# Kernel tuning notes

Measured on AMD Instinct MI355X. Metric: run time of the kernel, lower is better.

## Reference

```python
import jax, jax.numpy as jnp
import numpy as np

B, N, K = 4, 4096, 16
C_IN = 128
EPS = 1e-5


def setup_inputs() -> dict:
    key = jax.random.key(0)
    ks = jax.random.split(key, 8)
    c0 = 2 * C_IN + 3  # concat channels: pos_diff(3) + feat2(128) + feat1(128)
    return {
        "pos1": jax.random.normal(ks[0], (B, 3, N), jnp.float32),
        "pos2": jax.random.normal(ks[1], (B, 3, N), jnp.float32),
        "feature1": jax.random.normal(ks[2], (B, C_IN, N), jnp.float32),
        "feature2": jax.random.normal(ks[3], (B, C_IN, N), jnp.float32),
        "W0": jax.random.normal(ks[4], (128, c0), jnp.float32) * 0.05,
        "W1": jax.random.normal(ks[5], (128, 128), jnp.float32) * 0.05,
        "W2": jax.random.normal(ks[6], (128, 128), jnp.float32) * 0.05,
        "g0": jnp.ones((128,), jnp.float32),
        "g1": jnp.ones((128,), jnp.float32),
        "g2": jnp.ones((128,), jnp.float32),
        "b0": jnp.zeros((128,), jnp.float32),
        "b1": jnp.zeros((128,), jnp.float32),
        "b2": jnp.zeros((128,), jnp.float32),
    }


def _knn_idx(pos1, pos2, k):
    # pos1, pos2: (B, 3, N).  For each point in pos1, k nearest points in pos2.
    p1 = pos1.transpose(0, 2, 1)  # (B, N, 3)
    p2 = pos2.transpose(0, 2, 1)  # (B, M, 3)
    d = (jnp.sum(p1 * p1, -1, keepdims=True)
         + jnp.sum(p2 * p2, -1)[:, None, :]
         - 2.0 * jnp.einsum("bnc,bmc->bnm", p1, p2))  # (B, N, M) squared dists
    _, idx = jax.lax.top_k(-d, k)  # (B, N, K)
    return idx


def _group(x, idx):
    # x: (B, C, M), idx: (B, N, K) -> (B, C, N, K)
    xt = x.transpose(0, 2, 1)  # (B, M, C)
    g = jax.vmap(lambda a, i: a[i])(xt, idx)  # (B, N, K, C)
    return g.transpose(0, 3, 1, 2)


def _conv_bn_relu(x, W, g, b):
    # 1x1 conv (no bias) + BatchNorm2d (training: batch stats, biased var) + ReLU
    y = jnp.einsum("oc,bcnk->bonk", W, x)
    mu = jnp.mean(y, axis=(0, 2, 3), keepdims=True)
    var = jnp.var(y, axis=(0, 2, 3), keepdims=True)
    yn = (y - mu) * jax.lax.rsqrt(var + EPS)
    return jax.nn.relu(yn * g[None, :, None, None] + b[None, :, None, None])


def reference(pos1, pos2, feature1, feature2, W0, W1, W2, g0, g1, g2, b0, b1, b2):
    idx = _knn_idx(pos1, pos2, K)                      # (B, N, K)
    pos2_g = _group(pos2, idx)                         # (B, 3, N, K)
    pos_diff = pos2_g - pos1[:, :, :, None]
    feat2_g = _group(feature2, idx)                    # (B, C, N, K)
    feat1_rep = jnp.broadcast_to(feature1[:, :, :, None], (B, C_IN, N, K))
    x = jnp.concatenate([pos_diff, feat2_g, feat1_rep], axis=1)  # (B, 2C+3, N, K)
    x = _conv_bn_relu(x, W0, g0, b0)
    x = _conv_bn_relu(x, W1, g1, b1)
    x = _conv_bn_relu(x, W2, g2, b2)
    feat1_new = jnp.max(x, axis=-1)                    # (B, mlp[-1], N)
    return (pos1, feat1_new)
```

## Files before the change

kernel.cpp:

```cpp
#include <hip/hip_runtime.h>

#define B_ 4
#define N_ 4096
#define K_ 16
#define C_ 128
#define NQ (B_*N_)
#define COLS_TOT (NQ*K_)
#define CNT_F 262144.0f
#define EPS_ 1e-5f

typedef __attribute__((ext_vector_type(8))) short short8;
typedef __attribute__((ext_vector_type(4))) float f4;
typedef __attribute__((ext_vector_type(4))) int i4;
typedef unsigned long long u64;

__device__ __forceinline__ unsigned short f2bf(float f){
  unsigned u = __builtin_bit_cast(unsigned, f);
  u = u + 0x7fffu + ((u >> 16) & 1u);
  return (unsigned short)(u >> 16);
}
__device__ __forceinline__ float bf2f(unsigned short h){
  return __builtin_bit_cast(float, ((unsigned)h) << 16);
}
__device__ __forceinline__ int swzc(int c){ return c ^ ((c >> 3) & 7); }

__global__ __launch_bounds__(256) void knn_wconv(
    const float* __restrict__ pos1, const float* __restrict__ pos2,
    u64* __restrict__ kout,
    const float* __restrict__ W0, const float* __restrict__ W1,
    const float* __restrict__ W2,
    unsigned short* __restrict__ W0b, unsigned short* __restrict__ W0c,
    unsigned short* __restrict__ W1b, unsigned short* __restrict__ W2b)
{
  if (blockIdx.x >= 1024){
    int i = (blockIdx.x - 1024) * 256 + threadIdx.x;
    int sel = i >> 14, r = i & 16383;
    int o = r >> 7, c = r & 127;
    float v; unsigned short* dst;
    if (sel == 0)      { v = W0[o*259 + 3   + c]; dst = W0b; }
    else if (sel == 1) { v = W0[o*259 + 131 + c]; dst = W0c; }
    else if (sel == 2) { v = W1[o*128 + c];       dst = W1b; }
    else               { v = W2[o*128 + c];       dst = W2b; }
    dst[r] = f2bf(v);
    return;
  }
  __shared__ __align__(16) float pts[256*4];
  int bx = blockIdx.x;
  int b = bx >> 8, rest = bx & 255, ngrp = rest >> 4, chunk = rest & 15;
  int t = threadIdx.x;
  int m0 = chunk * 256;
  const float* p2 = pos2 + (size_t)b*3*N_;
  {
    int m = m0 + t;
    float x = p2[m], y = p2[N_ + m], z = p2[2*N_ + m];
    float sq = __fadd_rn(__fadd_rn(__fmul_rn(x,x), __fmul_rn(y,y)), __fmul_rn(z,z));
    f4 v; v.x = x; v.y = y; v.z = z; v.w = sq;
    *(f4*)(pts + t*4) = v;
  }
  __syncthreads();

  int n = ngrp*256 + t;
  const float* p1 = pos1 + (size_t)b*3*N_;
  float qx = p1[n], qy = p1[N_ + n], qz = p1[2*N_ + n];
  float qs = __fadd_rn(__fadd_rn(__fmul_rn(qx,qx), __fmul_rn(qy,qy)), __fmul_rn(qz,qz));

  u64 list[16];
  #pragma unroll
  for (int j = 0; j < 16; ++j) list[j] = ~0ull;

  #pragma unroll 1
  for (int tile = 0; tile < 16; ++tile){
    u64 tk[16];
    #pragma unroll
    for (int e = 0; e < 16; ++e){
      int it = tile*16 + e;
      f4 c = *(const f4*)(pts + it*4);
      float dot = __builtin_fmaf(qz, c.z,
                    __builtin_fmaf(qy, c.y, __fmul_rn(qx, c.x)));
      float d = __fsub_rn(__fadd_rn(qs, c.w), __fmul_rn(2.0f, dot));
      d = __fadd_rn(d, 0.0f);
      unsigned u = __builtin_bit_cast(unsigned, d);
      u ^= (unsigned)((int)u >> 31) | 0x80000000u;
      tk[e] = ((u64)u << 32) | (unsigned)(m0 + it);
    }
    #pragma unroll
    for (int k = 2; k <= 16; k <<= 1)
      #pragma unroll
      for (int j2 = k >> 1; j2 > 0; j2 >>= 1)
        #pragma unroll
        for (int i = 0; i < 16; ++i){
          int l = i ^ j2;
          if (l > i){
            bool up = ((i & k) == 0);
            u64 a = tk[i], bb = tk[l];
            bool sw = up ? (a > bb) : (a < bb);
            u64 lo = sw ? bb : a, hi = sw ? a : bb;
            tk[i] = lo; tk[l] = hi;
          }
        }
    u64 m16[16];
    #pragma unroll
    for (int i = 0; i < 16; ++i){
      u64 a = list[i], bb = tk[15 - i];
      m16[i] = a < bb ? a : bb;
    }
    #pragma unroll
    for (int j2 = 8; j2 > 0; j2 >>= 1)
      #pragma unroll
      for (int i = 0; i < 16; ++i){
        int l = i ^ j2;
        if (l > i){
          u64 a = m16[i], bb = m16[l];
          bool sw = a > bb;
          m16[i] = sw ? bb : a; m16[l] = sw ? a : bb;
        }
      }
    #pragma unroll
    for (int i = 0; i < 16; ++i) list[i] = m16[i];
  }

  int q = b*N_ + n;
  #pragma unroll
  for (int j = 0; j < 16; ++j)
    kout[(size_t)(chunk*16 + j)*NQ + q] = list[j];
}

__global__ __launch_bounds__(256) void merge_p1(
    const u64* __restrict__ kin, int* __restrict__ idxout,
    const float* __restrict__ feat2, const float* __restrict__ feat1,
    const unsigned short* __restrict__ W0b, const unsigned short* __restrict__ W0c,
    float* __restrict__ F2t, float* __restrict__ PREt)
{
  if (blockIdx.x < 64){
    int q = blockIdx.x*256 + threadIdx.x;
    u64 list[16];
    #pragma unroll
    for (int j = 0; j < 16; ++j) list[j] = ~0ull;
    #pragma unroll 1
    for (int l = 0; l < 16; ++l){
      u64 lv[16];
      #pragma unroll
      for (int j = 0; j < 16; ++j)
        lv[j] = kin[(size_t)(l*16 + j)*NQ + q];
      bool dead = false;
      #pragma unroll
      for (int j = 0; j < 16; ++j){
        bool ins = !dead && (list[15] > lv[j]);
        dead = !ins;
        if (__any(ins)){
          if (ins){
            u64 key = lv[j];
            bool cm = list[14] > key;
            list[15] = cm ? list[14] : key;
            #pragma unroll
            for (int jj = 14; jj >= 1; --jj){
              bool cj = cm;
              cm = list[jj-1] > key;
              list[jj] = cj ? (cm ? list[jj-1] : key) : list[jj];
            }
            list[0] = cm ? key : list[0];
          }
        }
      }
    }
    #pragma unroll
    for (int j = 0; j < 4; ++j){
      i4 v;
      v.x = (int)(list[j*4]   & 0xFFF); v.y = (int)(list[j*4+1] & 0xFFF);
      v.z = (int)(list[j*4+2] & 0xFFF); v.w = (int)(list[j*4+3] & 0xFFF);
      *(i4*)(idxout + (size_t)q*16 + j*4) = v;
    }
    return;
  }
  __shared__ __align__(16) unsigned short X[16*128*8];
  int bid = blockIdx.x - 64;
  int sel = bid >> 7;
  const float* src = sel ? feat1 : feat2;
  const unsigned short* W = sel ? W0c : W0b;
  float* dst = sel ? PREt : F2t;
  int c0 = (bid & 127) * 128;
  int b = c0 >> 12, mm0 = c0 & 4095;
  int t = threadIdx.x;
  {
    int colt = t & 127, chh = t >> 7;
    #pragma unroll 4
    for (int it = 0; it < 64; ++it){
      int ch = it*2 + chh;
      float v = src[((size_t)b*C_ + ch)*N_ + mm0 + colt];
      X[(ch >> 3)*1024 + swzc(colt)*8 + (ch & 7)] = f2bf(v);
    }
  }
  int lane = t & 63, w = t >> 6;
  int or0 = (w >> 1)*64, c0w = (w & 1)*64;
  int lr = lane & 15, lg = lane >> 4;
  short8 af[4][4];
  #pragma unroll
  for (int ks = 0; ks < 4; ++ks)
    #pragma unroll
    for (int i = 0; i < 4; ++i)
      af[ks][i] = *(const short8*)(W + (or0 + 16*i + lr)*128 + ks*32 + 8*lg);
  __syncthreads();

  f4 acc[4][4] = {};
  #pragma unroll
  for (int ks = 0; ks < 4; ++ks){
    short8 bfr[4];
    #pragma unroll
    for (int j = 0; j < 4; ++j)
      bfr[j] = *(const short8*)(X + (ks*4 + lg)*1024 + swzc(c0w + 16*j + lr)*8);
    #pragma unroll
    for (int i = 0; i < 4; ++i)
      #pragma unroll
      for (int j = 0; j < 4; ++j)
        acc[i][j] = __builtin_amdgcn_mfma_f32_16x16x32_bf16(af[ks][i], bfr[j], acc[i][j], 0, 0, 0);
  }
  #pragma unroll
  for (int i = 0; i < 4; ++i)
    #pragma unroll
    for (int j = 0; j < 4; ++j){
      int col = c0 + c0w + 16*j + lr;
      *(f4*)(dst + (size_t)col*C_ + or0 + 16*i + 4*lg) = acc[i][j];
    }
}

__global__ __launch_bounds__(256) void k3_stats(
    const float* __restrict__ pos1, const float* __restrict__ pos2,
    const float* __restrict__ W0, const int* __restrict__ idx,
    const float* __restrict__ F2t, const float* __restrict__ PREt,
    float* __restrict__ partials)
{
  __shared__ float w0a[384];
  __shared__ float ldsS[256];
  int t = threadIdx.x;
  for (int i = t; i < 384; i += 256) w0a[i] = W0[(i/3)*259 + (i%3)];
  __syncthreads();
  int cloc = t & 15, chg = t >> 4, ch0 = chg*8;
  float wx[8], wy[8], wz[8];
  #pragma unroll
  for (int e = 0; e < 8; ++e){
    wx[e] = w0a[(ch0+e)*3]; wy[e] = w0a[(ch0+e)*3+1]; wz[e] = w0a[(ch0+e)*3+2];
  }
  float s1[8] = {}, s2[8] = {};
  int base = blockIdx.x * 256;
  for (int it = 0; it < 16; ++it){
    int col = base + it*16 + cloc;
    int nabs = col >> 4;
    int b = nabs >> 12, n = nabs & 4095;
    int m = idx[col];
    float dx = pos2[(size_t)(b*3+0)*N_ + m] - pos1[(size_t)(b*3+0)*N_ + n];
    float dy = pos2[(size_t)(b*3+1)*N_ + m] - pos1[(size_t)(b*3+1)*N_ + n];
    float dz = pos2[(size_t)(b*3+2)*N_ + m] - pos1[(size_t)(b*3+2)*N_ + n];
    const float* f2 = F2t  + ((size_t)b*N_ + m)*C_ + ch0;
    const float* pr = PREt + ((size_t)b*N_ + n)*C_ + ch0;
    #pragma unroll
    for (int e = 0; e < 8; ++e){
      float y = f2[e] + pr[e];
      y = fmaf(wx[e], dx, y); y = fmaf(wy[e], dy, y); y = fmaf(wz[e], dz, y);
      s1[e] += y; s2[e] = fmaf(y, y, s2[e]);
    }
  }
  #pragma unroll
  for (int e = 0; e < 8; ++e){
    float a = s1[e], q = s2[e];
    #pragma unroll
    for (int sft = 1; sft < 16; sft <<= 1){ a += __shfl_xor(a, sft); q += __shfl_xor(q, sft); }
    if (cloc == 0){ ldsS[ch0 + e] = a; ldsS[128 + ch0 + e] = q; }
  }
  __syncthreads();
  partials[(size_t)blockIdx.x*256 + t] = ldsS[t];
}

__global__ __launch_bounds__(256) void redfin(
    const float* __restrict__ partials, float* __restrict__ partial2,
    const float* __restrict__ g, const float* __restrict__ bb,
    float* __restrict__ cA, float* __restrict__ cB,
    int* __restrict__ counter)
{
  __shared__ float sh[256];
  __shared__ int isLast;
  int t = threadIdx.x, blk = blockIdx.x, R = gridDim.x;
  float a = 0.f;
  int r0 = blk*32;
  #pragma unroll 4
  for (int i = 0; i < 32; ++i) a += partials[(size_t)(r0+i)*256 + t];
  partial2[(size_t)blk*256 + t] = a;
  __threadfence();
  if (t == 0){
    int old = atomicAdd(counter, 1);
    isLast = (old == R - 1);
  }
  __syncthreads();
  if (!isLast) return;
  __threadfence();
  float s = 0.f;
  for (int i = 0; i < R; ++i) s += partial2[(size_t)i*256 + t];
  sh[t] = s;
  __syncthreads();
  if (t < 128){
    float mu = sh[t] / CNT_F;
    float var = sh[128 + t] / CNT_F - mu*mu;
    float A = g[t] * rsqrtf(var + EPS_);
    cA[t] = A; cB[t] = bb[t] - mu*A;
  }
  if (t == 0) *counter = 0;
}

__global__ __launch_bounds__(256,2) void layer1_fused(
    const float* __restrict__ pos1, const float* __restrict__ pos2,
    const float* __restrict__ W0, const int* __restrict__ idx,
    const float* __restrict__ F2t, const float* __restrict__ PREt,
    unsigned short* __restrict__ ybuf,
    const unsigned short* __restrict__ Wbf,
    const float* __restrict__ cA, const float* __restrict__ cB,
    float* __restrict__ partials)
{
  __shared__ __align__(16) char lds[40960];
  unsigned short* X = (unsigned short*)lds;
  float* ldsA = (float*)(lds + 32768);
  float* ldsB = ldsA + 128;
  float* w0a  = ldsB + 128;
  float* ldsS = w0a + 384;
  int t = threadIdx.x;
  int c0 = blockIdx.x * 128;
  if (t < 128){ ldsA[t] = cA[t]; ldsB[t] = cB[t]; }
  for (int i = t; i < 384; i += 256) w0a[i] = W0[(i/3)*259 + (i%3)];
  ldsS[t] = 0.f; ldsS[256 + t] = 0.f;
  __syncthreads();

  int lane = t & 63, w = t >> 6;
  int or0 = (w >> 1)*64, c0w = (w & 1)*64;
  int lr = lane & 15, lg = lane >> 4;

  {
    int colL = t >> 1, half = t & 1;
    int col = c0 + colL;
    int nabs = col >> 4;
    int b = nabs >> 12, n = nabs & 4095;
    int m = idx[col];
    float dx = pos2[(size_t)(b*3+0)*N_ + m] - pos1[(size_t)(b*3+0)*N_ + n];
    float dy = pos2[(size_t)(b*3+1)*N_ + m] - pos1[(size_t)(b*3+1)*N_ + n];
    float dz = pos2[(size_t)(b*3+2)*N_ + m] - pos1[(size_t)(b*3+2)*N_ + n];
    const float* f2 = F2t  + ((size_t)b*N_ + m)*C_ + half*64;
    const float* pr = PREt + ((size_t)b*N_ + n)*C_ + half*64;
    int sc = swzc(colL);
    #pragma unroll
    for (int cc = 0; cc < 8; ++cc){
      int ch0 = half*64 + cc*8;
      f4 a0 = *(const f4*)(f2 + cc*8), a1 = *(const f4*)(f2 + cc*8 + 4);
      f4 b0 = *(const f4*)(pr + cc*8), b1 = *(const f4*)(pr + cc*8 + 4);
      short8 xv;
      #pragma unroll
      for (int e = 0; e < 8; ++e){
        int ch = ch0 + e;
        float fv = (e < 4 ? a0[e] : a1[e-4]);
        float pv = (e < 4 ? b0[e] : b1[e-4]);
        float y = fv + pv;
        y = fmaf(w0a[ch*3], dx, y); y = fmaf(w0a[ch*3+1], dy, y); y = fmaf(w0a[ch*3+2], dz, y);
        float v = fmaf(y, ldsA[ch], ldsB[ch]);
        v = v > 0.f ? v : 0.f;
        xv[e] = (short)f2bf(v);
      }
      *(short8*)(X + (ch0 >> 3)*1024 + sc*8) = xv;
    }
  }

  short8 af[4][4];
  #pragma unroll
  for (int ks = 0; ks < 4; ++ks)
    #pragma unroll
    for (int i = 0; i < 4; ++i)
      af[ks][i] = *(const short8*)(Wbf + (or0 + 16*i + lr)*128 + ks*32 + 8*lg);
  __syncthreads();

  f4 acc[4][4] = {};
  #pragma unroll
  for (int ks = 0; ks < 4; ++ks){
    short8 bfr[4];
    #pragma unroll
    for (int j = 0; j < 4; ++j)
      bfr[j] = *(const short8*)(X + (ks*4 + lg)*1024 + swzc(c0w + 16*j + lr)*8);
    #pragma unroll
    for (int i = 0; i < 4; ++i)
      #pragma unroll
      for (int j = 0; j < 4; ++j)
        acc[i][j] = __builtin_amdgcn_mfma_f32_16x16x32_bf16(af[ks][i], bfr[j], acc[i][j], 0, 0, 0);
  }

  #pragma unroll
  for (int i = 0; i < 4; ++i)
    #pragma unroll
    for (int e = 0; e < 4; ++e){
      float a0 = acc[i][0][e], a1 = acc[i][1][e], a2 = acc[i][2][e], a3 = acc[i][3][e];
      float s1 = (a0 + a1) + (a2 + a3);
      float s2 = (a0*a0 + a1*a1) + (a2*a2 + a3*a3);
      #pragma unroll
      for (int sft = 1; sft < 16; sft <<= 1){ s1 += __shfl_xor(s1, sft); s2 += __shfl_xor(s2, sft); }
      if (lr == 0){
        int o = or0 + 16*i + 4*lg + e;
        ldsS[(w & 1)*256 + o] = s1;
        ldsS[(w & 1)*256 + 128 + o] = s2;
      }
    }

  __syncthreads();
  unsigned short* OT = (unsigned short*)lds;
  #pragma unroll
  for (int i = 0; i < 4; ++i)
    #pragma unroll
    for (int j = 0; j < 4; ++j){
      int col = c0w + 16*j + lr;
      int o0 = or0 + 16*i + 4*lg;
      unsigned long long pv =
          (unsigned long long)f2bf(acc[i][j][0])
        | ((unsigned long long)f2bf(acc[i][j][1]) << 16)
        | ((unsigned long long)f2bf(acc[i][j][2]) << 32)
        | ((unsigned long long)f2bf(acc[i][j][3]) << 48);
      *(unsigned long long*)(OT + col*136 + o0) = pv;
    }
  __syncthreads();
  {
    int colL = t >> 1, half = t & 1;
    unsigned short* dst = ybuf + (size_t)(c0 + colL)*128 + half*64;
    #pragma unroll
    for (int cc = 0; cc < 8; ++cc){
      short8 v = *(const short8*)(OT + colL*136 + half*64 + cc*8);
      *(short8*)(dst + cc*8) = v;
    }
  }
  __syncthreads();
  partials[(size_t)blockIdx.x*256 + t] = ldsS[t] + ldsS[256 + t];
}

__global__ __launch_bounds__(256,2) void layer_gemm_last(
    unsigned short* ybuf,
    const unsigned short* __restrict__ Wbf,
    const float* __restrict__ cA, const float* __restrict__ cB,
    float* __restrict__ y2max,
    float* __restrict__ partials)
{
  __shared__ __align__(16) char lds[38912];
  unsigned short* X = (unsigned short*)lds;
  float* ldsA = (float*)(lds + 34816);
  float* ldsB = ldsA + 128;
  float* ldsS = ldsB + 128;
  int t = threadIdx.x;
  int c0 = blockIdx.x * 128;
  if (t < 128){ ldsA[t] = cA[t]; ldsB[t] = cB[t]; }
  ldsS[t] = 0.f; ldsS[256 + t] = 0.f;

  int lane = t & 63, w = t >> 6;
  int or0 = (w >> 1)*64, c0w = (w & 1)*64;
  int lr = lane & 15, lg = lane >> 4;
  short8 af[4][4];
  #pragma unroll
  for (int ks = 0; ks < 4; ++ks)
    #pragma unroll
    for (int i = 0; i < 4; ++i)
      af[ks][i] = *(const short8*)(Wbf + (or0 + 16*i + lr)*128 + ks*32 + 8*lg);
  __syncthreads();

  {
    int colL = t >> 1, half = t & 1;
    const unsigned short* src = ybuf + (size_t)(c0 + colL)*128 + half*64;
    int sc = swzc(colL);
    #pragma unroll
    for (int cc = 0; cc < 8; ++cc){
      int ch0 = half*64 + cc*8;
      short8 yv = *(const short8*)(src + cc*8);
      short8 xv;
      #pragma unroll
      for (int e = 0; e < 8; ++e){
        float f = bf2f((unsigned short)yv[e]);
        float v = fmaf(f, ldsA[ch0 + e], ldsB[ch0 + e]);
        v = v > 0.f ? v : 0.f;
        xv[e] = (short)f2bf(v);
      }
      *(short8*)(X + (ch0 >> 3)*1024 + sc*8) = xv;
    }
  }
  __syncthreads();

  f4 acc[4][4] = {};
  #pragma unroll
  for (int ks = 0; ks < 4; ++ks){
    short8 bfr[4];
    #pragma unroll
    for (int j = 0; j < 4; ++j)
      bfr[j] = *(const short8*)(X + (ks*4 + lg)*1024 + swzc(c0w + 16*j + lr)*8);
    #pragma unroll
    for (int i = 0; i < 4; ++i)
      #pragma unroll
      for (int j = 0; j < 4; ++j)
        acc[i][j] = __builtin_amdgcn_mfma_f32_16x16x32_bf16(af[ks][i], bfr[j], acc[i][j], 0, 0, 0);
  }

  #pragma unroll
  for (int i = 0; i < 4; ++i)
    #pragma unroll
    for (int e = 0; e < 4; ++e){
      float a0 = acc[i][0][e], a1 = acc[i][1][e], a2 = acc[i][2][e], a3 = acc[i][3][e];
      float s1 = (a0 + a1) + (a2 + a3);
      float s2 = (a0*a0 + a1*a1) + (a2*a2 + a3*a3);
      #pragma unroll
      for (int sft = 1; sft < 16; sft <<= 1){ s1 += __shfl_xor(s1, sft); s2 += __shfl_xor(s2, sft); }
      if (lr == 0){
        int o = or0 + 16*i + 4*lg + e;
        ldsS[(w & 1)*256 + o] = s1;
        ldsS[(w & 1)*256 + 128 + o] = s2;
      }
    }

  float keep[4][4] = {};
  #pragma unroll
  for (int j = 0; j < 4; ++j)
    #pragma unroll
    for (int i = 0; i < 4; ++i)
      #pragma unroll
      for (int e = 0; e < 4; ++e){
        float v = acc[i][j][e];
        #pragma unroll
        for (int sft = 1; sft < 16; sft <<= 1) v = fmaxf(v, __shfl_xor(v, sft));
        if (lr == j) keep[i][e] = v;
      }
  if (lr < 4){
    int colg = c0 + c0w + 16*lr;
    int nabs = colg >> 4;
    float* dst = y2max + (size_t)nabs*C_;
    #pragma unroll
    for (int i = 0; i < 4; ++i){
      f4 v; v.x = keep[i][0]; v.y = keep[i][1]; v.z = keep[i][2]; v.w = keep[i][3];
      *(f4*)(dst + or0 + 16*i + 4*lg) = v;
    }
  }
  __syncthreads();
  partials[(size_t)blockIdx.x*256 + t] = ldsS[t] + ldsS[256 + t];
}

__global__ __launch_bounds__(256) void k7_fat(
    const float* __restrict__ y2max, const float* __restrict__ cA,
    const float* __restrict__ cB, float* __restrict__ outF,
    const float* __restrict__ pos1, float* __restrict__ out0)
{
  if (blockIdx.x >= 256){
    int i = ((blockIdx.x - 256)*256 + threadIdx.x)*4;
    *(f4*)(out0 + i) = *(const f4*)(pos1 + i);
    return;
  }
  __shared__ __align__(16) float T[128*65];
  int t = threadIdx.x, bid = blockIdx.x;
  int b = bid >> 6, n0 = (bid & 63)*64;
  {
    int nl = t >> 2, o0 = (t & 3)*32;
    const float* src = y2max + ((size_t)b*N_ + n0 + nl)*C_ + o0;
    #pragma unroll
    for (int jj = 0; jj < 8; ++jj){
      f4 v = *(const f4*)(src + jj*4);
      T[(o0 + jj*4 + 0)*65 + nl] = v.x;
      T[(o0 + jj*4 + 1)*65 + nl] = v.y;
      T[(o0 + jj*4 + 2)*65 + nl] = v.z;
      T[(o0 + jj*4 + 3)*65 + nl] = v.w;
    }
  }
  __syncthreads();
  {
    int o = t >> 1, half = t & 1;
    float A = cA[o], Bb = cB[o];
    float* dst = outF + ((size_t)b*C_ + o)*N_ + n0 + half*32;
    #pragma unroll
    for (int jj = 0; jj < 8; ++jj){
      f4 v;
      float x0 = fmaf(T[o*65 + half*32 + jj*4+0], A, Bb);
      float x1 = fmaf(T[o*65 + half*32 + jj*4+1], A, Bb);
      float x2 = fmaf(T[o*65 + half*32 + jj*4+2], A, Bb);
      float x3 = fmaf(T[o*65 + half*32 + jj*4+3], A, Bb);
      v.x = x0 > 0.f ? x0 : 0.f; v.y = x1 > 0.f ? x1 : 0.f;
      v.z = x2 > 0.f ? x2 : 0.f; v.w = x3 > 0.f ? x3 : 0.f;
      *(f4*)(dst + jj*4) = v;
    }
  }
}

extern "C" void kernel_launch(void* const* d_in, const int* in_sizes, int n_in,
                              void* d_out, int out_size, void* d_ws, size_t ws_size,
                              hipStream_t stream)
{
  (void)in_sizes; (void)n_in; (void)out_size; (void)ws_size;
  const float* pos1  = (const float*)d_in[0];
  const float* pos2  = (const float*)d_in[1];
  const float* feat1 = (const float*)d_in[2];
  const float* feat2 = (const float*)d_in[3];
  const float* W0 = (const float*)d_in[4];
  const float* W1 = (const float*)d_in[5];
  const float* W2 = (const float*)d_in[6];
  const float* g0 = (const float*)d_in[7];
  const float* g1 = (const float*)d_in[8];
  const float* g2 = (const float*)d_in[9];
  const float* b0 = (const float*)d_in[10];
  const float* b1 = (const float*)d_in[11];
  const float* b2 = (const float*)d_in[12];

  char* ws = (char*)d_ws;
  size_t off = 0;
  auto alloc = [&](size_t bytes){ size_t r = off; off += (bytes + 255) & ~(size_t)255; return r; };
  int*   idx     = (int*)  (ws + alloc((size_t)COLS_TOT*4));
  float* F2t     = (float*)(ws + alloc((size_t)NQ*C_*4));
  float* PREt    = (float*)(ws + alloc((size_t)NQ*C_*4));
  unsigned short* ybuf = (unsigned short*)(ws + alloc((size_t)COLS_TOT*C_*2));
  float* y2max   = (float*)(ws + alloc((size_t)NQ*C_*4));
  float* partials= (float*)(ws + alloc((size_t)2048*256*4));
  float* partial2= (float*)(ws + alloc((size_t)64*256*4));
  float* coef    = (float*)(ws + alloc((size_t)6*128*4));
  int*   ctrs    = (int*)  (ws + alloc(256));
  unsigned short* W0bb = (unsigned short*)(ws + alloc(16384*2));
  unsigned short* W0cb = (unsigned short*)(ws + alloc(16384*2));
  unsigned short* W1b  = (unsigned short*)(ws + alloc(16384*2));
  unsigned short* W2b  = (unsigned short*)(ws + alloc(16384*2));

  u64* knn_k = (u64*)ybuf;

  float* cA0 = coef,       *cB0 = coef + 128;
  float* cA1 = coef + 256, *cB1 = coef + 384;
  float* cA2 = coef + 512, *cB2 = coef + 640;

  hipMemsetAsync(ctrs, 0, 256, stream);
  knn_wconv<<<1280, 256, 0, stream>>>(pos1, pos2, knn_k, W0, W1, W2,
                                       W0bb, W0cb, W1b, W2b);
  merge_p1<<<320, 256, 0, stream>>>(knn_k, idx, feat2, feat1, W0bb, W0cb, F2t, PREt);
  k3_stats<<<1024, 256, 0, stream>>>(pos1, pos2, W0, idx, F2t, PREt, partials);
  redfin<<<32, 256, 0, stream>>>(partials, partial2, g0, b0, cA0, cB0, ctrs + 0);
  layer1_fused<<<2048, 256, 0, stream>>>(pos1, pos2, W0, idx, F2t, PREt,
                                          ybuf, W1b, cA0, cB0, partials);
  redfin<<<64, 256, 0, stream>>>(partials, partial2, g1, b1, cA1, cB1, ctrs + 16);
  layer_gemm_last<<<2048, 256, 0, stream>>>(ybuf, W2b, cA1, cB1, y2max, partials);
  redfin<<<64, 256, 0, stream>>>(partials, partial2, g2, b2, cA2, cB2, ctrs + 32);
  k7_fat<<<304, 256, 0, stream>>>(y2max, cA2, cB2,
                                   (float*)d_out + (size_t)B_*3*N_, pos1, (float*)d_out);
}
```

Baseline: 361.4 us.

## Co-schedule feature GEMM with half the KNN blocks and split KNN launch

The KNN candidate search is split into two launches, each covering 8 of the 16 pos2 chunks. The first launch also carries the feature2/feature1 projection GEMM blocks and the W1/W2 bf16 conversion, so that GEMM work overlaps with KNN compute instead of running after it alongside the merge. The merge becomes its own small 64-block kernel. W0 is now converted to bf16 inline from fp32 inside the GEMM blocks, which removes two staging buffers. The cost is one extra kernel launch, and the merge now runs alone with low occupancy.

```diff
diff --git a/kernel.cpp b/kernel.cpp
--- a/kernel.cpp
+++ b/kernel.cpp
@@ -24,29 +24,85 @@
 }
 __device__ __forceinline__ int swzc(int c){ return c ^ ((c >> 3) & 7); }
 
-__global__ __launch_bounds__(256) void knn_wconv(
+template<int EXTRA>
+__global__ __launch_bounds__(256) void knn_fat(
     const float* __restrict__ pos1, const float* __restrict__ pos2,
-    u64* __restrict__ kout,
+    u64* __restrict__ kout, int chunk0,
     const float* __restrict__ W0, const float* __restrict__ W1,
     const float* __restrict__ W2,
-    unsigned short* __restrict__ W0b, unsigned short* __restrict__ W0c,
-    unsigned short* __restrict__ W1b, unsigned short* __restrict__ W2b)
-{
-  if (blockIdx.x >= 1024){
-    int i = (blockIdx.x - 1024) * 256 + threadIdx.x;
+    unsigned short* __restrict__ W1b, unsigned short* __restrict__ W2b,
+    const float* __restrict__ feat2, const float* __restrict__ feat1,
+    float* __restrict__ F2t, float* __restrict__ PREt)
+{
+  if (EXTRA && blockIdx.x >= 768){
+    int i = (blockIdx.x - 768) * 256 + threadIdx.x;
     int sel = i >> 14, r = i & 16383;
-    int o = r >> 7, c = r & 127;
-    float v; unsigned short* dst;
-    if (sel == 0)      { v = W0[o*259 + 3   + c]; dst = W0b; }
-    else if (sel == 1) { v = W0[o*259 + 131 + c]; dst = W0c; }
-    else if (sel == 2) { v = W1[o*128 + c];       dst = W1b; }
-    else               { v = W2[o*128 + c];       dst = W2b; }
-    dst[r] = f2bf(v);
+    const float* src = sel ? W2 : W1;
+    unsigned short* dst = sel ? W2b : W1b;
+    dst[r] = f2bf(src[r]);
+    return;
+  }
+  if (EXTRA && blockIdx.x >= 512){
+    __shared__ __align__(16) unsigned short X[16*128*8];
+    int bid = blockIdx.x - 512;
+    int sel = bid >> 7;
+    const float* src = sel ? feat1 : feat2;
+    float* dst = sel ? PREt : F2t;
+    int c0 = (bid & 127) * 128;
+    int b = c0 >> 12, mm0 = c0 & 4095;
+    int t = threadIdx.x;
+    {
+      int colt = t & 127, chh = t >> 7;
+      #pragma unroll 4
+      for (int it = 0; it < 64; ++it){
+        int ch = it*2 + chh;
+        float v = src[((size_t)b*C_ + ch)*N_ + mm0 + colt];
+        X[(ch >> 3)*1024 + swzc(colt)*8 + (ch & 7)] = f2bf(v);
+      }
+    }
+    int lane = t & 63, w = t >> 6;
+    int or0 = (w >> 1)*64, c0w = (w & 1)*64;
+    int lr = lane & 15, lg = lane >> 4;
+    short8 af[4][4];
+    #pragma unroll
+    for (int ks = 0; ks < 4; ++ks)
+      #pragma unroll
+      for (int i = 0; i < 4; ++i){
+        const float* wr = W0 + (size_t)(or0 + 16*i + lr)*259 + 3 + sel*128
+                             + ks*32 + 8*lg;
+        f4 lo = *(const f4*)wr, hi = *(const f4*)(wr + 4);
+        short8 v;
+        #pragma unroll
+        for (int e = 0; e < 4; ++e){ v[e] = (short)f2bf(lo[e]); v[e+4] = (short)f2bf(hi[e]); }
+        af[ks][i] = v;
+      }
+    __syncthreads();
+
+    f4 acc[4][4] = {};
+    #pragma unroll
+    for (int ks = 0; ks < 4; ++ks){
+      short8 bfr[4];
+      #pragma unroll
+      for (int j = 0; j < 4; ++j)
+        bfr[j] = *(const short8*)(X + (ks*4 + lg)*1024 + swzc(c0w + 16*j + lr)*8);
+      #pragma unroll
+      for (int i = 0; i < 4; ++i)
+        #pragma unroll
+        for (int j = 0; j < 4; ++j)
+          acc[i][j] = __builtin_amdgcn_mfma_f32_16x16x32_bf16(af[ks][i], bfr[j], acc[i][j], 0, 0, 0);
+    }
+    #pragma unroll
+    for (int i = 0; i < 4; ++i)
+      #pragma unroll
+      for (int j = 0; j < 4; ++j){
+        int col = c0 + c0w + 16*j + lr;
+        *(f4*)(dst + (size_t)col*C_ + or0 + 16*i + 4*lg) = acc[i][j];
+      }
     return;
   }
   __shared__ __align__(16) float pts[256*4];
   int bx = blockIdx.x;
-  int b = bx >> 8, rest = bx & 255, ngrp = rest >> 4, chunk = rest & 15;
+  int b = bx >> 7, rest = bx & 127, ngrp = rest >> 3, chunk = chunk0 + (rest & 7);
   int t = threadIdx.x;
   int m0 = chunk * 256;
   const float* p2 = pos2 + (size_t)b*3*N_;
@@ -125,102 +181,47 @@
     kout[(size_t)(chunk*16 + j)*NQ + q] = list[j];
 }
 
-__global__ __launch_bounds__(256) void merge_p1(
-    const u64* __restrict__ kin, int* __restrict__ idxout,
-    const float* __restrict__ feat2, const float* __restrict__ feat1,
-    const unsigned short* __restrict__ W0b, const unsigned short* __restrict__ W0c,
-    float* __restrict__ F2t, float* __restrict__ PREt)
-{
-  if (blockIdx.x < 64){
-    int q = blockIdx.x*256 + threadIdx.x;
-    u64 list[16];
-    #pragma unroll
-    for (int j = 0; j < 16; ++j) list[j] = ~0ull;
-    #pragma unroll 1
-    for (int l = 0; l < 16; ++l){
-      u64 lv[16];
-      #pragma unroll
-      for (int j = 0; j < 16; ++j)
-        lv[j] = kin[(size_t)(l*16 + j)*NQ + q];
-      bool dead = false;
-      #pragma unroll
-      for (int j = 0; j < 16; ++j){
-        bool ins = !dead && (list[15] > lv[j]);
-        dead = !ins;
-        if (__any(ins)){
-          if (ins){
-            u64 key = lv[j];
-            bool cm = list[14] > key;
-            list[15] = cm ? list[14] : key;
-            #pragma unroll
-            for (int jj = 14; jj >= 1; --jj){
-              bool cj = cm;
-              cm = list[jj-1] > key;
-              list[jj] = cj ? (cm ? list[jj-1] : key) : list[jj];
-            }
-            list[0] = cm ? key : list[0];
+__global__ __launch_bounds__(256) void knn_merge(
+    const u64* __restrict__ kin, int* __restrict__ idxout)
+{
+  int q = blockIdx.x*256 + threadIdx.x;
+  u64 list[16];
+  #pragma unroll
+  for (int j = 0; j < 16; ++j) list[j] = ~0ull;
+  #pragma unroll 1
+  for (int l = 0; l < 16; ++l){
+    u64 lv[16];
+    #pragma unroll
+    for (int j = 0; j < 16; ++j)
+      lv[j] = kin[(size_t)(l*16 + j)*NQ + q];
+    bool dead = false;
+    #pragma unroll
+    for (int j = 0; j < 16; ++j){
+      bool ins = !dead && (list[15] > lv[j]);
+      dead = !ins;
+      if (__any(ins)){
+        if (ins){
+          u64 key = lv[j];
+          bool cm = list[14] > key;
+          list[15] = cm ? list[14] : key;
+          #pragma unroll
+          for (int jj = 14; jj >= 1; --jj){
+            bool cj = cm;
+            cm = list[jj-1] > key;
+            list[jj] = cj ? (cm ? list[jj-1] : key) : list[jj];
           }
+          list[0] = cm ? key : list[0];
         }
       }
     }
-    #pragma unroll
-    for (int j = 0; j < 4; ++j){
-      i4 v;
-      v.x = (int)(list[j*4]   & 0xFFF); v.y = (int)(list[j*4+1] & 0xFFF);
-      v.z = (int)(list[j*4+2] & 0xFFF); v.w = (int)(list[j*4+3] & 0xFFF);
-      *(i4*)(idxout + (size_t)q*16 + j*4) = v;
-    }
-    return;
-  }
-  __shared__ __align__(16) unsigned short X[16*128*8];
-  int bid = blockIdx.x - 64;
-  int sel = bid >> 7;
-  const float* src = sel ? feat1 : feat2;
-  const unsigned short* W = sel ? W0c : W0b;
-  float* dst = sel ? PREt : F2t;
-  int c0 = (bid & 127) * 128;
-  int b = c0 >> 12, mm0 = c0 & 4095;
-  int t = threadIdx.x;
-  {
-    int colt = t & 127, chh = t >> 7;
-    #pragma unroll 4
-    for (int it = 0; it < 64; ++it){
-      int ch = it*2 + chh;
-      float v = src[((size_t)b*C_ + ch)*N_ + mm0 + colt];
-      X[(ch >> 3)*1024 + swzc(colt)*8 + (ch & 7)] = f2bf(v);
-    }
-  }
-  int lane = t & 63, w = t >> 6;
-  int or0 = (w >> 1)*64, c0w = (w & 1)*64;
-  int lr = lane & 15, lg = lane >> 4;
-  short8 af[4][4];
-  #pragma unroll
-  for (int ks = 0; ks < 4; ++ks)
-    #pragma unroll
-    for (int i = 0; i < 4; ++i)
-      af[ks][i] = *(const short8*)(W + (or0 + 16*i + lr)*128 + ks*32 + 8*lg);
-  __syncthreads();
-
-  f4 acc[4][4] = {};
-  #pragma unroll
-  for (int ks = 0; ks < 4; ++ks){
-    short8 bfr[4];
-    #pragma unroll
-    for (int j = 0; j < 4; ++j)
-      bfr[j] = *(const short8*)(X + (ks*4 + lg)*1024 + swzc(c0w + 16*j + lr)*8);
-    #pragma unroll
-    for (int i = 0; i < 4; ++i)
-      #pragma unroll
-      for (int j = 0; j < 4; ++j)
-        acc[i][j] = __builtin_amdgcn_mfma_f32_16x16x32_bf16(af[ks][i], bfr[j], acc[i][j], 0, 0, 0);
-  }
-  #pragma unroll
-  for (int i = 0; i < 4; ++i)
-    #pragma unroll
-    for (int j = 0; j < 4; ++j){
-      int col = c0 + c0w + 16*j + lr;
-      *(f4*)(dst + (size_t)col*C_ + or0 + 16*i + 4*lg) = acc[i][j];
-    }
+  }
+  #pragma unroll
+  for (int j = 0; j < 4; ++j){
+    i4 v;
+    v.x = (int)(list[j*4]   & 0xFFF); v.y = (int)(list[j*4+1] & 0xFFF);
+    v.z = (int)(list[j*4+2] & 0xFFF); v.w = (int)(list[j*4+3] & 0xFFF);
+    *(i4*)(idxout + (size_t)q*16 + j*4) = v;
+  }
 }
 
 __global__ __launch_bounds__(256) void k3_stats(
@@ -611,8 +612,6 @@
   float* partial2= (float*)(ws + alloc((size_t)64*256*4));
   float* coef    = (float*)(ws + alloc((size_t)6*128*4));
   int*   ctrs    = (int*)  (ws + alloc(256));
-  unsigned short* W0bb = (unsigned short*)(ws + alloc(16384*2));
-  unsigned short* W0cb = (unsigned short*)(ws + alloc(16384*2));
   unsigned short* W1b  = (unsigned short*)(ws + alloc(16384*2));
   unsigned short* W2b  = (unsigned short*)(ws + alloc(16384*2));
 
@@ -623,9 +622,11 @@
   float* cA2 = coef + 512, *cB2 = coef + 640;
 
   hipMemsetAsync(ctrs, 0, 256, stream);
-  knn_wconv<<<1280, 256, 0, stream>>>(pos1, pos2, knn_k, W0, W1, W2,
-                                       W0bb, W0cb, W1b, W2b);
-  merge_p1<<<320, 256, 0, stream>>>(knn_k, idx, feat2, feat1, W0bb, W0cb, F2t, PREt);
+  knn_fat<1><<<896, 256, 0, stream>>>(pos1, pos2, knn_k, 0, W0, W1, W2,
+                                       W1b, W2b, feat2, feat1, F2t, PREt);
+  knn_fat<0><<<512, 256, 0, stream>>>(pos1, pos2, knn_k, 8, W0, W1, W2,
+                                       W1b, W2b, feat2, feat1, F2t, PREt);
+  knn_merge<<<64, 256, 0, stream>>>(knn_k, idx);
   k3_stats<<<1024, 256, 0, stream>>>(pos1, pos2, W0, idx, F2t, PREt, partials);
   redfin<<<32, 256, 0, stream>>>(partials, partial2, g0, b0, cA0, cB0, ctrs + 0);
   layer1_fused<<<2048, 256, 0, stream>>>(pos1, pos2, W0, idx, F2t, PREt,
```

New measurement: 370.9 us. 2.6% more time.
